# Optimization experiments

Hardware: AMD Instinct MI355X
Metric: run time of the kernel (lower is better)

Reference implementation:

```python
import jax, jax.numpy as jnp
import numpy as np

N = 100000
E = 1600000
F_IN = 32
H = 64
EDGE_DIM = 2
OUT = 1
NEG_SLOPE = 0.2


def setup_inputs() -> dict:
    key = jax.random.key(0)
    ks = jax.random.split(key, 20)
    g = lambda k, shape, fan_in: jax.random.normal(k, shape, jnp.float32) / np.sqrt(fan_in)
    inp = {
        "x": jax.random.normal(ks[0], (N, F_IN), jnp.float32),
        "edge_index": jax.random.randint(ks[1], (2, E), 0, N, jnp.int32),
        "edge_attr": jax.random.normal(ks[2], (E, EDGE_DIM), jnp.float32),
        # GATConv layer 1 (in=F_IN, out=H, heads=1, edge_dim=EDGE_DIM)
        "W1": g(ks[3], (F_IN, H), F_IN),
        "as1": g(ks[4], (H,), H),
        "ad1": g(ks[5], (H,), H),
        "We1": g(ks[6], (EDGE_DIM, H), EDGE_DIM),
        "ae1": g(ks[7], (H,), H),
        "b1": jnp.zeros((H,), jnp.float32),
        # GATConv layer 2 (in=H, out=H)
        "W2": g(ks[8], (H, H), H),
        "as2": g(ks[9], (H,), H),
        "ad2": g(ks[10], (H,), H),
        "We2": g(ks[11], (EDGE_DIM, H), EDGE_DIM),
        "ae2": g(ks[12], (H,), H),
        "b2": jnp.zeros((H,), jnp.float32),
        # Linear head
        "Wl": g(ks[13], (H, OUT), H),
        "bl": jnp.zeros((OUT,), jnp.float32),
    }
    return inp


def gat_conv(x, src, dst, edge_attr, W, att_src, att_dst, We, att_e, bias):
    """PyG GATConv, heads=1, add_self_loops=True (fill_value='mean'), eval mode."""
    n = x.shape[0]
    # add self-loops; self-loop edge_attr = mean of edge_attr (fill_value='mean')
    loop_attr = jnp.mean(edge_attr, axis=0)
    src_a = jnp.concatenate([src, jnp.arange(n, dtype=src.dtype)])
    dst_a = jnp.concatenate([dst, jnp.arange(n, dtype=dst.dtype)])
    ea = jnp.concatenate([edge_attr, jnp.broadcast_to(loop_attr, (n, edge_attr.shape[1]))])
    h = x @ W                          # [n, H]
    a_src = h @ att_src                # [n]
    a_dst = h @ att_dst                # [n]
    a_edge = (ea @ We) @ att_e         # [E+n]
    alpha = a_src[src_a] + a_dst[dst_a] + a_edge
    alpha = jax.nn.leaky_relu(alpha, NEG_SLOPE)
    # segment softmax over incoming edges of each destination node
    amax = jax.ops.segment_max(alpha, dst_a, num_segments=n)
    ex = jnp.exp(alpha - amax[dst_a])
    denom = jax.ops.segment_sum(ex, dst_a, num_segments=n)
    w = ex / denom[dst_a]              # every node has a self-loop -> denom > 0
    out = jax.ops.segment_sum(h[src_a] * w[:, None], dst_a, num_segments=n)
    return out + bias


def reference(x, edge_index, edge_attr, W1, as1, ad1, We1, ae1, b1,
              W2, as2, ad2, We2, ae2, b2, Wl, bl):
    src, dst = edge_index[0], edge_index[1]
    h = gat_conv(x, src, dst, edge_attr, W1, as1, ad1, We1, ae1, b1)
    h = jax.nn.relu(h)  # dropout is identity in eval mode
    h = gat_conv(h, src, dst, edge_attr, W2, as2, ad2, We2, ae2, b2)
    h = h @ Wl + bl
    return jax.nn.relu(h)
```

## Files before the change

### kernel.cpp

```cpp
#include <hip/hip_runtime.h>
#include <hip/hip_fp16.h>
#include <cstdint>

#define HH 64
#define NEG 0.2f
#define NB 256
#define SH 7
#define BKCAP 1024
#define ECAP 4096
#define CHCAP 6272

__device__ __forceinline__ float leaky(float x){ return x > 0.f ? x : NEG * x; }

__global__ void k_hist(const int* __restrict__ dst, const float* __restrict__ ea,
                       int* __restrict__ ghist, float2* __restrict__ pbuf,
                       int E, int nbkt, int CH){
    __shared__ int hist[BKCAP];
    __shared__ float2 sm[8];
    for (int i = threadIdx.x; i < nbkt; i += 512) hist[i] = 0;
    __syncthreads();
    int b = blockIdx.x;
    int e0 = b * CH, e1 = min(E, e0 + CH);
    float s0 = 0.f, s1 = 0.f;
    for (int e = e0 + threadIdx.x; e < e1; e += 512){
        int d = dst[e];
        atomicAdd(&hist[d >> SH], 1);
        float2 v = *reinterpret_cast<const float2*>(ea + 2ll * e);
        s0 += v.x; s1 += v.y;
    }
    #pragma unroll
    for (int o = 32; o; o >>= 1){ s0 += __shfl_xor(s0, o); s1 += __shfl_xor(s1, o); }
    int wv = threadIdx.x >> 6;
    if ((threadIdx.x & 63) == 0) sm[wv] = make_float2(s0, s1);
    __syncthreads();
    if (threadIdx.x == 0){
        float m0 = 0.f, m1 = 0.f;
        #pragma unroll
        for (int i = 0; i < 8; ++i){ m0 += sm[i].x; m1 += sm[i].y; }
        pbuf[b] = make_float2(m0, m1);
    }
    for (int i = threadIdx.x; i < nbkt; i += 512)
        ghist[(size_t)b * nbkt + i] = hist[i];
}

__global__ void k_const(const float* __restrict__ We1, const float* __restrict__ ae1,
                        const float* __restrict__ We2, const float* __restrict__ ae2,
                        const float2* __restrict__ pbuf, float* __restrict__ cbuf,
                        float invE, int nbp){
    int k = threadIdx.x;
    float m0 = 0.f, m1 = 0.f;
    for (int i = k; i < nbp; i += 64){ float2 u = pbuf[i]; m0 += u.x; m1 += u.y; }
    float p0 = We1[k] * ae1[k], p1 = We1[64 + k] * ae1[k];
    float q0 = We2[k] * ae2[k], q1 = We2[64 + k] * ae2[k];
    #pragma unroll
    for (int o = 32; o; o >>= 1){
        m0 += __shfl_xor(m0, o); m1 += __shfl_xor(m1, o);
        p0 += __shfl_xor(p0, o); p1 += __shfl_xor(p1, o);
        q0 += __shfl_xor(q0, o); q1 += __shfl_xor(q1, o);
    }
    if (k == 0){
        m0 *= invE; m1 *= invE;
        cbuf[4] = p0; cbuf[5] = p1; cbuf[6] = q0; cbuf[7] = q1;
        cbuf[2] = m0 * p0 + m1 * p1;
        cbuf[3] = m0 * q0 + m1 * q1;
    }
}

__global__ void k_scanA(const int* __restrict__ ghist, int* __restrict__ incl,
                        int* __restrict__ part, int M, int nbkt){
    __shared__ int sm[256];
    int tid = threadIdx.x;
    int i = blockIdx.x * 256 + tid;
    int v = 0;
    if (i < M) v = ghist[(size_t)(i % NB) * nbkt + (i / NB)];
    int x = v;
    sm[tid] = x; __syncthreads();
    for (int o = 1; o < 256; o <<= 1){
        int t = (tid >= o) ? sm[tid - o] : 0;
        __syncthreads();
        x += t; sm[tid] = x;
        __syncthreads();
    }
    if (i < M) incl[i] = x;
    if (tid == 255) part[blockIdx.x] = x;
}

__global__ void k_scanB(int* __restrict__ part, int nb){
    __shared__ int sm[1024];
    int tid = threadIdx.x;
    int C = (nb + 1023) >> 10;
    if (C > 8) C = 8;
    int base = tid * C;
    int vals[8];
    int s = 0;
    #pragma unroll
    for (int k = 0; k < 8; ++k){
        if (k < C){
            int i = base + k;
            int v = (i < nb) ? part[i] : 0;
            vals[k] = v; s += v;
        }
    }
    sm[tid] = s; __syncthreads();
    int x = s;
    for (int o = 1; o < 1024; o <<= 1){
        int t = (tid >= o) ? sm[tid - o] : 0;
        __syncthreads();
        x += t; sm[tid] = x;
        __syncthreads();
    }
    int excl = x - s;
    #pragma unroll
    for (int k = 0; k < 8; ++k){
        if (k < C){
            int i = base + k;
            if (i < nb){ int v = vals[k]; part[i] = excl; excl += v; }
        }
    }
}

__global__ void k_scanC(const int* __restrict__ ghist, const int* __restrict__ incl,
                        const int* __restrict__ part, int* __restrict__ gbase,
                        int M, int nbkt){
    int i = blockIdx.x * 256 + threadIdx.x;
    if (i < M){
        int v = ghist[(size_t)(i % NB) * nbkt + (i / NB)];
        gbase[i] = part[blockIdx.x] + incl[i] - v;
    }
}

__global__ void k_scatter2(const int* __restrict__ src, const int* __restrict__ dst,
                           const float* __restrict__ ea, const int* __restrict__ ghist,
                           const int* __restrict__ gbase, const float* __restrict__ cbuf,
                           uint2* __restrict__ csort, int E, int nbkt, int CH){
    __shared__ uint2 srec[CHCAP];
    __shared__ unsigned short bktof[CHCAP];
    __shared__ int gb[BKCAP];
    __shared__ int cur[BKCAP];
    __shared__ int wsum[512];
    int tid = threadIdx.x;
    int b = blockIdx.x;
    int base2 = tid * 2;
    int v0 = 0, v1 = 0;
    if (base2 < nbkt)     v0 = ghist[(size_t)b * nbkt + base2];
    if (base2 + 1 < nbkt) v1 = ghist[(size_t)b * nbkt + base2 + 1];
    int s = v0 + v1;
    wsum[tid] = s; __syncthreads();
    int x = s;
    for (int o = 1; o < 512; o <<= 1){
        int t = (tid >= o) ? wsum[tid - o] : 0;
        __syncthreads();
        x += t; wsum[tid] = x;
        __syncthreads();
    }
    int excl = x - s;
    if (base2 < nbkt)     cur[base2]     = excl;
    if (base2 + 1 < nbkt) cur[base2 + 1] = excl + v0;
    __syncthreads();
    for (int i = tid; i < nbkt; i += 512)
        gb[i] = gbase[(size_t)i * NB + b] - cur[i];
    __syncthreads();
    float c4 = cbuf[4], c5 = cbuf[5], c6 = cbuf[6], c7 = cbuf[7];
    int e0 = b * CH, e1 = min(E, e0 + CH);
    for (int e = e0 + tid; e < e1; e += 512){
        int d = dst[e];
        int bkt = d >> SH;
        float2 v = *reinterpret_cast<const float2*>(ea + 2ll * e);
        float a1 = v.x * c4 + v.y * c5;
        float a2 = v.x * c6 + v.y * c7;
        __half2 ah = __floats2half2_rn(a1, a2);
        int p = atomicAdd(&cur[bkt], 1);
        uint2 o;
        o.x = (unsigned)src[e] | ((unsigned)(d & ((1 << SH) - 1)) << 20);
        o.y = *reinterpret_cast<unsigned*>(&ah);
        srec[p] = o;
        bktof[p] = (unsigned short)bkt;
    }
    __syncthreads();
    int cnt = e1 - e0;
    for (int j = tid; j < cnt; j += 512)
        csort[gb[bktof[j]] + j] = srec[j];
}

template<int F, bool HALFIN>
__global__ void k_feat(const void* __restrict__ inp, const float* __restrict__ W,
                       const float* __restrict__ as_, const float* __restrict__ ad_,
                       __half* __restrict__ h, float* __restrict__ asrc,
                       float* __restrict__ adst, int n){
    int lane = threadIdx.x & 63;
    int wid0 = (blockIdx.x * blockDim.x + threadIdx.x) >> 6;
    int nw   = (gridDim.x * blockDim.x) >> 6;
    float wcol[F];
    #pragma unroll
    for (int i = 0; i < F; ++i) wcol[i] = W[i * HH + lane];
    float asl = as_[lane], adl = ad_[lane];
    for (int wid = wid0; wid < n; wid += nw){
        int u = __builtin_amdgcn_readfirstlane(wid);
        float a0 = 0.f, a1 = 0.f, a2 = 0.f, a3 = 0.f;
        if constexpr (!HALFIN){
            const float* __restrict__ row = (const float*)inp + (size_t)u * F;
            #pragma unroll
            for (int i = 0; i < F; i += 4){
                a0 += row[i]     * wcol[i];
                a1 += row[i + 1] * wcol[i + 1];
                a2 += row[i + 2] * wcol[i + 2];
                a3 += row[i + 3] * wcol[i + 3];
            }
        } else {
            const unsigned* __restrict__ row =
                (const unsigned*)((const __half*)inp + (size_t)u * F);
            #pragma unroll
            for (int i = 0; i < F / 2; i += 2){
                unsigned p0 = row[i], p1 = row[i + 1];
                __half2 h0 = *reinterpret_cast<__half2*>(&p0);
                __half2 h1 = *reinterpret_cast<__half2*>(&p1);
                float2 f0 = __half22float2(h0), f1 = __half22float2(h1);
                a0 += f0.x * wcol[2 * i];
                a1 += f0.y * wcol[2 * i + 1];
                a2 += f1.x * wcol[2 * i + 2];
                a3 += f1.y * wcol[2 * i + 3];
            }
        }
        float acc = (a0 + a1) + (a2 + a3);
        h[(size_t)u * HH + lane] = __float2half(acc);
        float vs = acc * asl, vd = acc * adl;
        #pragma unroll
        for (int o = 32; o; o >>= 1){ vs += __shfl_xor(vs, o); vd += __shfl_xor(vd, o); }
        if (lane == 0){ asrc[u] = vs; adst[u] = vd; }
    }
}

template<int AFIELD, bool RELU, bool HEAD>
__global__ void __launch_bounds__(256) k_fused4(
        const __half* __restrict__ h, const uint2* __restrict__ csort,
        const int* __restrict__ gbase, const float* __restrict__ asrc,
        const float* __restrict__ adst, const float* __restrict__ cbuf,
        const float* __restrict__ bias, const float* __restrict__ Wl,
        const float* __restrict__ bl, __half* __restrict__ outh,
        float* __restrict__ outf, int E, int n, int nbkt){
    __shared__ uint2 srec[ECAP];
    __shared__ int nhist[128], sscan[128], ncur[128];
    int tid = threadIdx.x, bkt = blockIdx.x;
    int base = gbase[(size_t)bkt * NB];
    int end  = (bkt + 1 < nbkt) ? gbase[(size_t)(bkt + 1) * NB] : E;
    int cnt  = min(end - base, ECAP);
    int node0 = bkt << SH;
    if (tid < 128) nhist[tid] = 0;
    __syncthreads();
    for (int j = tid; j < cnt; j += 256){
        uint2 r = csort[base + j];
        atomicAdd(&nhist[(r.x >> 20) & 127], 1);
    }
    __syncthreads();
    int v = (tid < 128) ? nhist[tid] : 0;
    if (tid < 128) sscan[tid] = v;
    __syncthreads();
    for (int o = 1; o < 128; o <<= 1){
        int t = 0;
        if (tid < 128 && tid >= o) t = sscan[tid - o];
        __syncthreads();
        if (tid < 128) sscan[tid] += t;
        __syncthreads();
    }
    if (tid < 128) ncur[tid] = sscan[tid] - v;
    __syncthreads();
    for (int j = tid; j < cnt; j += 256){
        uint2 r = csort[base + j];
        int p = atomicAdd(&ncur[(r.x >> 20) & 127], 1);
        srec[p] = r;
    }
    __syncthreads();

    int g = tid >> 3, l7 = tid & 7;
    float cself = cbuf[AFIELD == 1 ? 2 : 3];
    auto pick = [](uint2 rr) -> float {
        __half2 ah = *reinterpret_cast<const __half2*>(&rr.y);
        return (AFIELD == 1) ? __low2float(ah) : __high2float(ah);
    };
    #pragma unroll
    for (int rd = 0; rd < 4; ++rd){
        int nl = g + rd * 32;
        int node = node0 + nl;
        if (node >= n) continue;
        int ke = sscan[nl];
        int kb = ke - nhist[nl];
        float ad = adst[node];
        float aself = leaky(asrc[node] + ad + cself);
        float exs = __expf(aself);
        float dsum = exs;
        float acc[8];
        {
            float4 q = *reinterpret_cast<const float4*>(h + (size_t)node * HH + (l7 << 3));
            const __half2* ph = reinterpret_cast<const __half2*>(&q);
            #pragma unroll
            for (int i = 0; i < 4; ++i){
                float2 f = __half22float2(ph[i]);
                acc[2 * i]     = exs * f.x;
                acc[2 * i + 1] = exs * f.y;
            }
        }
        int k = kb;
        for (; k + 3 < ke; k += 4){
            uint2 r0 = srec[k], r1 = srec[k + 1], r2 = srec[k + 2], r3 = srec[k + 3];
            int s0 = r0.x & 0xFFFFF, s1 = r1.x & 0xFFFFF;
            int s2 = r2.x & 0xFFFFF, s3 = r3.x & 0xFFFFF;
            float w0 = __expf(leaky(asrc[s0] + ad + pick(r0)));
            float w1 = __expf(leaky(asrc[s1] + ad + pick(r1)));
            float w2 = __expf(leaky(asrc[s2] + ad + pick(r2)));
            float w3 = __expf(leaky(asrc[s3] + ad + pick(r3)));
            dsum += (w0 + w1) + (w2 + w3);
            float4 q0 = *reinterpret_cast<const float4*>(h + (size_t)s0 * HH + (l7 << 3));
            float4 q1 = *reinterpret_cast<const float4*>(h + (size_t)s1 * HH + (l7 << 3));
            float4 q2 = *reinterpret_cast<const float4*>(h + (size_t)s2 * HH + (l7 << 3));
            float4 q3 = *reinterpret_cast<const float4*>(h + (size_t)s3 * HH + (l7 << 3));
            const __half2* p0 = reinterpret_cast<const __half2*>(&q0);
            const __half2* p1 = reinterpret_cast<const __half2*>(&q1);
            const __half2* p2 = reinterpret_cast<const __half2*>(&q2);
            const __half2* p3 = reinterpret_cast<const __half2*>(&q3);
            #pragma unroll
            for (int i = 0; i < 4; ++i){
                float2 f0 = __half22float2(p0[i]);
                float2 f1 = __half22float2(p1[i]);
                float2 f2 = __half22float2(p2[i]);
                float2 f3 = __half22float2(p3[i]);
                acc[2 * i]     += w0 * f0.x + w1 * f1.x + w2 * f2.x + w3 * f3.x;
                acc[2 * i + 1] += w0 * f0.y + w1 * f1.y + w2 * f2.y + w3 * f3.y;
            }
        }
        for (; k < ke; ++k){
            uint2 rr = srec[k];
            int s = rr.x & 0xFFFFF;
            float w = __expf(leaky(asrc[s] + ad + pick(rr)));
            dsum += w;
            float4 q = *reinterpret_cast<const float4*>(h + (size_t)s * HH + (l7 << 3));
            const __half2* ph = reinterpret_cast<const __half2*>(&q);
            #pragma unroll
            for (int i = 0; i < 4; ++i){
                float2 f = __half22float2(ph[i]);
                acc[2 * i]     += w * f.x;
                acc[2 * i + 1] += w * f.y;
            }
        }
        float inv = 1.f / dsum;
        float4 b0 = *reinterpret_cast<const float4*>(bias + (l7 << 3));
        float4 b1 = *reinterpret_cast<const float4*>(bias + (l7 << 3) + 4);
        float r[8];
        r[0] = acc[0] * inv + b0.x; r[1] = acc[1] * inv + b0.y;
        r[2] = acc[2] * inv + b0.z; r[3] = acc[3] * inv + b0.w;
        r[4] = acc[4] * inv + b1.x; r[5] = acc[5] * inv + b1.y;
        r[6] = acc[6] * inv + b1.z; r[7] = acc[7] * inv + b1.w;
        if (RELU){
            #pragma unroll
            for (int i = 0; i < 8; ++i) r[i] = fmaxf(r[i], 0.f);
        }
        if (!HEAD){
            __half2 q01 = __floats2half2_rn(r[0], r[1]);
            __half2 q23 = __floats2half2_rn(r[2], r[3]);
            __half2 q45 = __floats2half2_rn(r[4], r[5]);
            __half2 q67 = __floats2half2_rn(r[6], r[7]);
            uint4 st;
            st.x = *reinterpret_cast<unsigned*>(&q01);
            st.y = *reinterpret_cast<unsigned*>(&q23);
            st.z = *reinterpret_cast<unsigned*>(&q45);
            st.w = *reinterpret_cast<unsigned*>(&q67);
            *reinterpret_cast<uint4*>(outh + (size_t)node * HH + (l7 << 3)) = st;
        } else {
            float4 w0 = *reinterpret_cast<const float4*>(Wl + (l7 << 3));
            float4 w1 = *reinterpret_cast<const float4*>(Wl + (l7 << 3) + 4);
            float vv = r[0] * w0.x + r[1] * w0.y + r[2] * w0.z + r[3] * w0.w
                     + r[4] * w1.x + r[5] * w1.y + r[6] * w1.z + r[7] * w1.w;
            vv += __shfl_xor(vv, 1); vv += __shfl_xor(vv, 2); vv += __shfl_xor(vv, 4);
            if (l7 == 0) outf[node] = fmaxf(vv + bl[0], 0.f);
        }
    }
}

extern "C" void kernel_launch(void* const* d_in, const int* in_sizes, int n_in,
                              void* d_out, int out_size, void* d_ws, size_t ws_size,
                              hipStream_t stream) {
    const float* x   = (const float*)d_in[0];
    const int*   ei  = (const int*)  d_in[1];
    const float* ea  = (const float*)d_in[2];
    const float* W1  = (const float*)d_in[3];
    const float* as1 = (const float*)d_in[4];
    const float* ad1 = (const float*)d_in[5];
    const float* We1 = (const float*)d_in[6];
    const float* ae1 = (const float*)d_in[7];
    const float* b1  = (const float*)d_in[8];
    const float* W2  = (const float*)d_in[9];
    const float* as2 = (const float*)d_in[10];
    const float* ad2 = (const float*)d_in[11];
    const float* We2 = (const float*)d_in[12];
    const float* ae2 = (const float*)d_in[13];
    const float* b2  = (const float*)d_in[14];
    const float* Wl  = (const float*)d_in[15];
    const float* bl  = (const float*)d_in[16];
    float* out = (float*)d_out;

    const int N = in_sizes[0] / 32;
    const int E = in_sizes[1] / 2;
    const int* srcI = ei;
    const int* dstI = ei + E;

    const int nbkt = (N + (1 << SH) - 1) >> SH;
    const int M    = nbkt * NB;
    const int CH   = (E + NB - 1) / NB;
    const int gMs  = (M + 255) / 256;

    char* ws = (char*)d_ws;
    size_t off = 0;
    auto alloc = [&](size_t bytes)->char*{
        char* p = ws + off;
        off += (bytes + 255) & ~size_t(255);
        return p;
    };
    __half*  hbuf   = (__half*) alloc((size_t)N * HH * 2);
    __half*  bufB   = (__half*) alloc((size_t)N * HH * 2);
    uint2*   csort  = (uint2*)  alloc((size_t)E * 8);
    int*     ghist  = (int*)    alloc((size_t)M * 4);
    int*     incl   = (int*)    alloc((size_t)M * 4);
    int*     gbase  = (int*)    alloc((size_t)M * 4);
    int*     part   = (int*)    alloc((size_t)gMs * 4);
    float*   asrc   = (float*)  alloc((size_t)N * 4);
    float*   adst   = (float*)  alloc((size_t)N * 4);
    float2*  pbuf   = (float2*) alloc((size_t)NB * 8);
    float*   cbuf   = (float*)  alloc(64);
    if (off > ws_size) return;

    const int BLK = 256;

    k_hist<<<NB, 512, 0, stream>>>(dstI, ea, ghist, pbuf, E, nbkt, CH);
    k_const<<<1, 64, 0, stream>>>(We1, ae1, We2, ae2, pbuf, cbuf, 1.f / (float)E, NB);
    k_scanA<<<gMs, 256, 0, stream>>>(ghist, incl, part, M, nbkt);
    k_scanB<<<1, 1024, 0, stream>>>(part, gMs);
    k_scanC<<<gMs, 256, 0, stream>>>(ghist, incl, part, gbase, M, nbkt);
    k_scatter2<<<NB, 512, 0, stream>>>(srcI, dstI, ea, ghist, gbase, cbuf, csort, E, nbkt, CH);

    k_feat<32, false><<<2048, BLK, 0, stream>>>(x, W1, as1, ad1, hbuf, asrc, adst, N);
    k_fused4<1, true, false><<<nbkt, BLK, 0, stream>>>(hbuf, csort, gbase, asrc, adst,
                                                       cbuf, b1, nullptr, nullptr,
                                                       bufB, nullptr, E, N, nbkt);

    k_feat<64, true><<<2048, BLK, 0, stream>>>(bufB, W2, as2, ad2, hbuf, asrc, adst, N);
    k_fused4<2, false, true><<<nbkt, BLK, 0, stream>>>(hbuf, csort, gbase, asrc, adst,
                                                       cbuf, b2, Wl, bl,
                                                       nullptr, out, E, N, nbkt);
}
```

Measured before the change: 175.4 us.

## Double histogram/scatter blocks, merge constant kernel into scan, unroll gather by 8

Doubles the number of blocks used by the histogram and scatter passes, which halves the per-block edge chunk, and shrinks the chunk and edge capacities to match. Folds the small constant-computation kernel into a second block of the scanB kernel to save one launch. Unrolls the neighbor aggregation loop from 4 to 8 edges per iteration, issuing all record, weight and feature loads before accumulating, to expose more memory-level parallelism. The costs are a larger per-bucket histogram (twice as many partial counts to scan) and higher register pressure in the fused aggregation kernel.

```diff
diff --git a/kernel.cpp b/kernel.cpp
--- a/kernel.cpp
+++ b/kernel.cpp
@@ -4,11 +4,11 @@
 
 #define HH 64
 #define NEG 0.2f
-#define NB 256
+#define NB 512
 #define SH 7
 #define BKCAP 1024
-#define ECAP 4096
-#define CHCAP 6272
+#define ECAP 2560
+#define CHCAP 3200
 
 __device__ __forceinline__ float leaky(float x){ return x > 0.f ? x : NEG * x; }
 
@@ -41,29 +41,6 @@
     }
     for (int i = threadIdx.x; i < nbkt; i += 512)
         ghist[(size_t)b * nbkt + i] = hist[i];
-}
-
-__global__ void k_const(const float* __restrict__ We1, const float* __restrict__ ae1,
-                        const float* __restrict__ We2, const float* __restrict__ ae2,
-                        const float2* __restrict__ pbuf, float* __restrict__ cbuf,
-                        float invE, int nbp){
-    int k = threadIdx.x;
-    float m0 = 0.f, m1 = 0.f;
-    for (int i = k; i < nbp; i += 64){ float2 u = pbuf[i]; m0 += u.x; m1 += u.y; }
-    float p0 = We1[k] * ae1[k], p1 = We1[64 + k] * ae1[k];
-    float q0 = We2[k] * ae2[k], q1 = We2[64 + k] * ae2[k];
-    #pragma unroll
-    for (int o = 32; o; o >>= 1){
-        m0 += __shfl_xor(m0, o); m1 += __shfl_xor(m1, o);
-        p0 += __shfl_xor(p0, o); p1 += __shfl_xor(p1, o);
-        q0 += __shfl_xor(q0, o); q1 += __shfl_xor(q1, o);
-    }
-    if (k == 0){
-        m0 *= invE; m1 *= invE;
-        cbuf[4] = p0; cbuf[5] = p1; cbuf[6] = q0; cbuf[7] = q1;
-        cbuf[2] = m0 * p0 + m1 * p1;
-        cbuf[3] = m0 * q0 + m1 * q1;
-    }
 }
 
 __global__ void k_scanA(const int* __restrict__ ghist, int* __restrict__ incl,
@@ -85,7 +62,33 @@
     if (tid == 255) part[blockIdx.x] = x;
 }
 
-__global__ void k_scanB(int* __restrict__ part, int nb){
+__global__ void k_scanB(int* __restrict__ part, int nb,
+                        const float* __restrict__ We1, const float* __restrict__ ae1,
+                        const float* __restrict__ We2, const float* __restrict__ ae2,
+                        const float2* __restrict__ pbuf, float* __restrict__ cbuf,
+                        float invE, int nbp){
+    if (blockIdx.x == 1){
+        int k = threadIdx.x;
+        if (k < 64){
+            float m0 = 0.f, m1 = 0.f;
+            for (int i = k; i < nbp; i += 64){ float2 u = pbuf[i]; m0 += u.x; m1 += u.y; }
+            float p0 = We1[k] * ae1[k], p1 = We1[64 + k] * ae1[k];
+            float q0 = We2[k] * ae2[k], q1 = We2[64 + k] * ae2[k];
+            #pragma unroll
+            for (int o = 32; o; o >>= 1){
+                m0 += __shfl_xor(m0, o); m1 += __shfl_xor(m1, o);
+                p0 += __shfl_xor(p0, o); p1 += __shfl_xor(p1, o);
+                q0 += __shfl_xor(q0, o); q1 += __shfl_xor(q1, o);
+            }
+            if (k == 0){
+                m0 *= invE; m1 *= invE;
+                cbuf[4] = p0; cbuf[5] = p1; cbuf[6] = q0; cbuf[7] = q1;
+                cbuf[2] = m0 * p0 + m1 * p1;
+                cbuf[3] = m0 * q0 + m1 * q1;
+            }
+        }
+        return;
+    }
     __shared__ int sm[1024];
     int tid = threadIdx.x;
     int C = (nb + 1023) >> 10;
@@ -300,31 +303,31 @@
             }
         }
         int k = kb;
-        for (; k + 3 < ke; k += 4){
-            uint2 r0 = srec[k], r1 = srec[k + 1], r2 = srec[k + 2], r3 = srec[k + 3];
-            int s0 = r0.x & 0xFFFFF, s1 = r1.x & 0xFFFFF;
-            int s2 = r2.x & 0xFFFFF, s3 = r3.x & 0xFFFFF;
-            float w0 = __expf(leaky(asrc[s0] + ad + pick(r0)));
-            float w1 = __expf(leaky(asrc[s1] + ad + pick(r1)));
-            float w2 = __expf(leaky(asrc[s2] + ad + pick(r2)));
-            float w3 = __expf(leaky(asrc[s3] + ad + pick(r3)));
-            dsum += (w0 + w1) + (w2 + w3);
-            float4 q0 = *reinterpret_cast<const float4*>(h + (size_t)s0 * HH + (l7 << 3));
-            float4 q1 = *reinterpret_cast<const float4*>(h + (size_t)s1 * HH + (l7 << 3));
-            float4 q2 = *reinterpret_cast<const float4*>(h + (size_t)s2 * HH + (l7 << 3));
-            float4 q3 = *reinterpret_cast<const float4*>(h + (size_t)s3 * HH + (l7 << 3));
-            const __half2* p0 = reinterpret_cast<const __half2*>(&q0);
-            const __half2* p1 = reinterpret_cast<const __half2*>(&q1);
-            const __half2* p2 = reinterpret_cast<const __half2*>(&q2);
-            const __half2* p3 = reinterpret_cast<const __half2*>(&q3);
-            #pragma unroll
-            for (int i = 0; i < 4; ++i){
-                float2 f0 = __half22float2(p0[i]);
-                float2 f1 = __half22float2(p1[i]);
-                float2 f2 = __half22float2(p2[i]);
-                float2 f3 = __half22float2(p3[i]);
-                acc[2 * i]     += w0 * f0.x + w1 * f1.x + w2 * f2.x + w3 * f3.x;
-                acc[2 * i + 1] += w0 * f0.y + w1 * f1.y + w2 * f2.y + w3 * f3.y;
+        for (; k + 7 < ke; k += 8){
+            uint2 rr[8];
+            #pragma unroll
+            for (int u = 0; u < 8; ++u) rr[u] = srec[k + u];
+            float w[8];
+            #pragma unroll
+            for (int u = 0; u < 8; ++u){
+                int s = rr[u].x & 0xFFFFF;
+                w[u] = __expf(leaky(asrc[s] + ad + pick(rr[u])));
+            }
+            float4 q[8];
+            #pragma unroll
+            for (int u = 0; u < 8; ++u)
+                q[u] = *reinterpret_cast<const float4*>(
+                    h + (size_t)(rr[u].x & 0xFFFFF) * HH + (l7 << 3));
+            #pragma unroll
+            for (int u = 0; u < 8; ++u){
+                dsum += w[u];
+                const __half2* ph = reinterpret_cast<const __half2*>(&q[u]);
+                #pragma unroll
+                for (int i = 0; i < 4; ++i){
+                    float2 f = __half22float2(ph[i]);
+                    acc[2 * i]     += w[u] * f.x;
+                    acc[2 * i + 1] += w[u] * f.y;
+                }
             }
         }
         for (; k < ke; ++k){
@@ -430,9 +433,9 @@
     const int BLK = 256;
 
     k_hist<<<NB, 512, 0, stream>>>(dstI, ea, ghist, pbuf, E, nbkt, CH);
-    k_const<<<1, 64, 0, stream>>>(We1, ae1, We2, ae2, pbuf, cbuf, 1.f / (float)E, NB);
     k_scanA<<<gMs, 256, 0, stream>>>(ghist, incl, part, M, nbkt);
-    k_scanB<<<1, 1024, 0, stream>>>(part, gMs);
+    k_scanB<<<2, 1024, 0, stream>>>(part, gMs, We1, ae1, We2, ae2, pbuf, cbuf,
+                                    1.f / (float)E, NB);
     k_scanC<<<gMs, 256, 0, stream>>>(ghist, incl, part, gbase, M, nbkt);
     k_scatter2<<<NB, 512, 0, stream>>>(srcI, dstI, ea, ghist, gbase, cbuf, csort, E, nbkt, CH);
 
```

After: 206.3 us. 1.18x slower.
